# Performance work log

Measured on AMD Instinct MI355X. Metric: run time of the kernel, lower is better.

Reference implementation:

```python
import jax, jax.numpy as jnp
import numpy as np

B, L, D, H, K = 4, 2048, 1024, 16, 3
HEAD_DIM = D // H
LN_EPS = 1e-5


def setup_inputs() -> dict:
    key = jax.random.key(0)
    ks = jax.random.split(key, 12)
    w = lambda k, shp: jax.random.normal(k, shp, jnp.float32) * (shp[-1] ** -0.5)
    return {
        "x": jax.random.normal(ks[0], (B, L, D), jnp.float32),
        "band_importance": jax.random.normal(ks[1], (1, L), jnp.float32) * 0.02,
        "Wq": w(ks[2], (D, D)), "bq": jnp.zeros((D,), jnp.float32),
        "Wk": w(ks[3], (D, D)), "bk": jnp.zeros((D,), jnp.float32),
        "Wv": w(ks[4], (D, D)), "bv": jnp.zeros((D,), jnp.float32),
        "Wo": w(ks[5], (D, D)), "bo": jnp.zeros((D,), jnp.float32),
        "gamma": jnp.ones((D,), jnp.float32),
        "beta": jnp.zeros((D,), jnp.float32),
    }


def reference(x, band_importance, Wq, bq, Wk, bk, Wv, bv, Wo, bo, gamma, beta):
    Bx, Lx, Dx = x.shape
    hd = Dx // H
    # top-k over softmax(band_importance); PyTorch bool attn_mask: True = BLOCKED
    imp = jax.nn.softmax(band_importance, axis=-1)[0]            # (L,)
    _, idx = jax.lax.top_k(imp, K)                               # (K,) int
    col_mask = jnp.zeros((Lx,), bool).at[idx].set(True)          # (L,) True -> masked out
    bias = jnp.where(col_mask, -jnp.inf, 0.0).astype(x.dtype)    # (L,)

    q = (x @ Wq.T + bq).reshape(Bx, Lx, H, hd)
    k_ = (x @ Wk.T + bk).reshape(Bx, Lx, H, hd)
    v = (x @ Wv.T + bv).reshape(Bx, Lx, H, hd)

    scale = 1.0 / np.sqrt(hd)
    scores = jnp.einsum("bqhd,bkhd->bhqk", q, k_) * scale + bias[None, None, None, :]
    attn = jax.nn.softmax(scores, axis=-1)                       # (B,H,L,L)
    ctx = jnp.einsum("bhqk,bkhd->bqhd", attn, v).reshape(Bx, Lx, Dx)
    attn_out = ctx @ Wo.T + bo

    y = x + attn_out                                             # residual
    mu = jnp.mean(y, axis=-1, keepdims=True)
    var = jnp.mean((y - mu) ** 2, axis=-1, keepdims=True)
    return (y - mu) * jax.lax.rsqrt(var + LN_EPS) * gamma + beta
```

## Files before the change

### kernel.cpp

```cpp
#include <hip/hip_runtime.h>

#define GAS __attribute__((address_space(1)))
#define LAS __attribute__((address_space(3)))

typedef __attribute__((ext_vector_type(8))) short short8;
typedef __attribute__((ext_vector_type(4))) float f32x4;
typedef __attribute__((ext_vector_type(16))) float f32x16;
typedef __attribute__((ext_vector_type(4))) unsigned int u32x4;

#define MFMA16(a,b,c) __builtin_amdgcn_mfma_f32_16x16x32_bf16(a,b,c,0,0,0)
#define MFMA32(a,b,c) __builtin_amdgcn_mfma_f32_32x32x16_bf16(a,b,c,0,0,0)

__device__ __forceinline__ unsigned short f2b(float f) {
  unsigned u = __float_as_uint(f);
  u += 0x7fffu + ((u >> 16) & 1u);
  return (unsigned short)(u >> 16);
}
__device__ __forceinline__ float b2f(unsigned short h) {
  return __uint_as_float(((unsigned)h) << 16);
}
__device__ __forceinline__ unsigned cvtpk(float a, float b) {
  unsigned r;
  asm("v_cvt_pk_bf16_f32 %0, %1, %2" : "=v"(r) : "v"(a), "v"(b));
  return r;
}
__device__ __forceinline__ void pl32swap(unsigned &x, unsigned &y) {
  auto r = __builtin_amdgcn_permlane32_swap((int)x, (int)y, false, false);
  x = (unsigned)r[0]; y = (unsigned)r[1];
}
__device__ __forceinline__ float xhalf_sum(float v) {
  auto r = __builtin_amdgcn_permlane32_swap(__float_as_int(v), __float_as_int(v), false, false);
  return __int_as_float(r[0]) + __int_as_float(r[1]);
}
__device__ __forceinline__ float fexp2(float x) {
  float r;
  asm("v_exp_f32 %0, %1" : "=v"(r) : "v"(x));
  return r;
}

union FW { u32x4 u; short8 s; };

__global__ void cvt_all(const float* __restrict__ x,
                        const float* __restrict__ Wq, const float* __restrict__ Wk,
                        const float* __restrict__ Wv, const float* __restrict__ Wo,
                        unsigned short* __restrict__ xb,
                        unsigned short* __restrict__ Wqkvb,
                        unsigned short* __restrict__ Wob) {
  const int bid = blockIdx.x;
  const float* src;
  unsigned short* dst;
  int idx;
  if (bid < 8192) {
    src = x; dst = xb; idx = bid * 256 + threadIdx.x;
  } else {
    int wb = bid - 8192;
    int seg = wb >> 10;
    idx = (wb & 1023) * 256 + threadIdx.x;
    src = (seg == 0) ? Wq : (seg == 1) ? Wk : (seg == 2) ? Wv : Wo;
    dst = (seg == 3) ? Wob : (Wqkvb + (size_t)seg * 1048576);
  }
  float4 v = reinterpret_cast<const float4*>(src)[idx];
  ushort4 o;
  o.x = f2b(v.x); o.y = f2b(v.y); o.z = f2b(v.z); o.w = f2b(v.w);
  reinterpret_cast<ushort4*>(dst)[idx] = o;
}

__global__ void topk_idx(const float* __restrict__ band, int* __restrict__ idxout) {
  __shared__ float svals[256];
  __shared__ int   sidx[256];
  __shared__ int   chosen[3];
  const int t = threadIdx.x;
  for (int pass = 0; pass < 3; ++pass) {
    float best = -INFINITY; int bi = 1 << 30;
    for (int j = t; j < 2048; j += 256) {
      float v = band[j];
      bool skip = false;
      for (int p2 = 0; p2 < pass; ++p2) skip |= (chosen[p2] == j);
      if (!skip && (v > best || (v == best && j < bi))) { best = v; bi = j; }
    }
    svals[t] = best; sidx[t] = bi;
    __syncthreads();
    for (int s = 128; s > 0; s >>= 1) {
      if (t < s) {
        float v2 = svals[t + s]; int i2 = sidx[t + s];
        if (v2 > svals[t] || (v2 == svals[t] && i2 < sidx[t])) { svals[t] = v2; sidx[t] = i2; }
      }
      __syncthreads();
    }
    if (t == 0) chosen[pass] = sidx[0];
    __syncthreads();
  }
  if (t < 3) idxout[t] = chosen[t];
}

__global__ __launch_bounds__(256) void gemm_qkv(
    const unsigned short* __restrict__ A,
    const unsigned short* __restrict__ Wqkv,
    const float* __restrict__ bq, const float* __restrict__ bk,
    const float* __restrict__ bv,
    unsigned short* __restrict__ qout, unsigned short* __restrict__ kout,
    unsigned short* __restrict__ vout, float qscale)
{
  __shared__ short As[128][64];
  __shared__ short Bs[128][64];
  const int tid = threadIdx.x;
  const int w = tid >> 6, lane = tid & 63;
  const int wm = w >> 1, wn = w & 1;
  const int flat = blockIdx.y * 64 + blockIdx.x;
  const int swb = (flat & 7) * 192 + (flat >> 3);
  const int m0 = (swb & 63) * 128, n0 = (swb >> 6) * 128;
  const int rA = lane >> 3, cA = lane & 7;

  const int seg = n0 >> 10;
  const float* biasp = (seg == 0) ? bq : (seg == 1) ? bk : bv;
  unsigned short* outp = (seg == 0) ? qout : (seg == 1) ? kout : vout;
  const float scale = (seg == 0) ? qscale : 1.0f;

  f32x4 acc[4][4];
  #pragma unroll
  for (int mt = 0; mt < 4; ++mt)
    #pragma unroll
    for (int nt = 0; nt < 4; ++nt)
      #pragma unroll
      for (int r = 0; r < 4; ++r) acc[mt][nt][r] = 0.f;

  for (int kt = 0; kt < 16; ++kt) {
    #pragma unroll
    for (int j = 0; j < 4; ++j) {
      int r = w * 32 + j * 8;
      const unsigned short* ga = A + (size_t)(m0 + r + rA) * 1024 + kt * 64 + cA * 8;
      __builtin_amdgcn_global_load_lds((const GAS void*)ga, (LAS void*)&As[r][0], 16, 0, 0);
      const unsigned short* gb = Wqkv + (size_t)(n0 + r + rA) * 1024 + kt * 64 + cA * 8;
      __builtin_amdgcn_global_load_lds((const GAS void*)gb, (LAS void*)&Bs[r][0], 16, 0, 0);
    }
    __syncthreads();
    #pragma unroll
    for (int kc = 0; kc < 2; ++kc) {
      short8 a[4], b[4];
      #pragma unroll
      for (int mt = 0; mt < 4; ++mt)
        a[mt] = *reinterpret_cast<const short8*>(
            &As[wm * 64 + mt * 16 + (lane & 15)][kc * 32 + (lane >> 4) * 8]);
      #pragma unroll
      for (int nt = 0; nt < 4; ++nt)
        b[nt] = *reinterpret_cast<const short8*>(
            &Bs[wn * 64 + nt * 16 + (lane & 15)][kc * 32 + (lane >> 4) * 8]);
      __builtin_amdgcn_s_setprio(1);
      #pragma unroll
      for (int mt = 0; mt < 4; ++mt)
        #pragma unroll
        for (int nt = 0; nt < 4; ++nt)
          acc[mt][nt] = MFMA16(a[mt], b[nt], acc[mt][nt]);
      __builtin_amdgcn_s_setprio(0);
    }
    __syncthreads();
  }
  #pragma unroll
  for (int nt = 0; nt < 4; ++nt) {
    int col = n0 + wn * 64 + nt * 16 + (lane & 15);
    int coll = col & 1023;
    float bval = biasp[coll];
    int h_ = coll >> 6, d_ = coll & 63;
    #pragma unroll
    for (int mt = 0; mt < 4; ++mt) {
      int rbase = m0 + wm * 64 + mt * 16 + ((lane >> 4) << 2);
      #pragma unroll
      for (int r = 0; r < 4; ++r) {
        unsigned short val = f2b((acc[mt][nt][r] + bval) * scale);
        int row = rbase + r;
        int b_ = row >> 11, lt_ = row & 2047;
        outp[(((size_t)(b_ * 16 + h_)) * 2048 + lt_) * 64 + d_] = val;
      }
    }
  }
}

__global__ __launch_bounds__(256) void gemm_wo(
    const unsigned short* __restrict__ A,
    const unsigned short* __restrict__ Bw,
    const float* __restrict__ bias,
    unsigned short* __restrict__ C)
{
  __shared__ short As[128][64];
  __shared__ short Bs[128][64];
  const int tid = threadIdx.x;
  const int w = tid >> 6, lane = tid & 63;
  const int wm = w >> 1, wn = w & 1;
  const int flat = blockIdx.y * 64 + blockIdx.x;
  const int swb = (flat & 7) * 64 + (flat >> 3);
  const int m0 = (swb & 63) * 128, n0 = (swb >> 6) * 128;
  const int rA = lane >> 3, cA = lane & 7;

  f32x4 acc[4][4];
  #pragma unroll
  for (int mt = 0; mt < 4; ++mt)
    #pragma unroll
    for (int nt = 0; nt < 4; ++nt)
      #pragma unroll
      for (int r = 0; r < 4; ++r) acc[mt][nt][r] = 0.f;

  for (int kt = 0; kt < 16; ++kt) {
    #pragma unroll
    for (int j = 0; j < 4; ++j) {
      int r = w * 32 + j * 8;
      const unsigned short* ga = A + (size_t)(m0 + r + rA) * 1024 + kt * 64 + cA * 8;
      __builtin_amdgcn_global_load_lds((const GAS void*)ga, (LAS void*)&As[r][0], 16, 0, 0);
      const unsigned short* gb = Bw + (size_t)(n0 + r + rA) * 1024 + kt * 64 + cA * 8;
      __builtin_amdgcn_global_load_lds((const GAS void*)gb, (LAS void*)&Bs[r][0], 16, 0, 0);
    }
    __syncthreads();
    #pragma unroll
    for (int kc = 0; kc < 2; ++kc) {
      short8 a[4], b[4];
      #pragma unroll
      for (int mt = 0; mt < 4; ++mt)
        a[mt] = *reinterpret_cast<const short8*>(
            &As[wm * 64 + mt * 16 + (lane & 15)][kc * 32 + (lane >> 4) * 8]);
      #pragma unroll
      for (int nt = 0; nt < 4; ++nt)
        b[nt] = *reinterpret_cast<const short8*>(
            &Bs[wn * 64 + nt * 16 + (lane & 15)][kc * 32 + (lane >> 4) * 8]);
      __builtin_amdgcn_s_setprio(1);
      #pragma unroll
      for (int mt = 0; mt < 4; ++mt)
        #pragma unroll
        for (int nt = 0; nt < 4; ++nt)
          acc[mt][nt] = MFMA16(a[mt], b[nt], acc[mt][nt]);
      __builtin_amdgcn_s_setprio(0);
    }
    __syncthreads();
  }
  #pragma unroll
  for (int nt = 0; nt < 4; ++nt) {
    int col = n0 + wn * 64 + nt * 16 + (lane & 15);
    float bval = bias[col];
    #pragma unroll
    for (int mt = 0; mt < 4; ++mt) {
      int rbase = m0 + wm * 64 + mt * 16 + ((lane >> 4) << 2);
      #pragma unroll
      for (int r = 0; r < 4; ++r)
        C[(size_t)(rbase + r) * 1024 + col] = f2b(acc[mt][nt][r] + bval);
    }
  }
}

__global__ __launch_bounds__(256) void transpose_v(
    const unsigned short* __restrict__ vin,
    unsigned short* __restrict__ vout)
{
  __shared__ short T[64 * 64];
  const int lt = blockIdx.x, bh = blockIdx.y;
  const int tid = threadIdx.x;
  #pragma unroll
  for (int p = 0; p < 2; ++p) {
    int id = p * 256 + tid; int l = id >> 3, c = id & 7;
    short8 v = *reinterpret_cast<const short8*>(
        vin + ((size_t)bh * 2048 + lt * 64 + l) * 64 + c * 8);
    *reinterpret_cast<short8*>(&T[l * 64 + ((c ^ (l & 7)) * 8)]) = v;
  }
  __syncthreads();
  #pragma unroll
  for (int p = 0; p < 2; ++p) {
    int id = p * 256 + tid; int d = id >> 3, c2 = id & 7;
    short8 o;
    #pragma unroll
    for (int j = 0; j < 8; ++j) {
      int l = c2 * 8 + j;
      o[j] = T[l * 64 + (((d >> 3) ^ (l & 7)) * 8) + (d & 7)];
    }
    *reinterpret_cast<short8*>(vout + ((size_t)bh * 64 + d) * 2048 + lt * 64 + c2 * 8) = o;
  }
}

#define PACK8(S, j0, OUT) {                                        \
    unsigned A_ = cvtpk(S[(j0)+0], S[(j0)+1]);                     \
    unsigned B_ = cvtpk(S[(j0)+4], S[(j0)+5]);                     \
    unsigned C_ = cvtpk(S[(j0)+2], S[(j0)+3]);                     \
    unsigned D_ = cvtpk(S[(j0)+6], S[(j0)+7]);                     \
    pl32swap(A_, B_); pl32swap(C_, D_);                            \
    FW f_; f_.u[0] = A_; f_.u[1] = C_; f_.u[2] = B_; f_.u[3] = D_; \
    OUT = f_.s; }

__global__ __launch_bounds__(256, 3) void attn4(
    const unsigned short* __restrict__ qg,
    const unsigned short* __restrict__ kg,
    const unsigned short* __restrict__ vtg,
    const int* __restrict__ midx,
    unsigned short* __restrict__ ctx)
{
  __shared__ short Ks[2][64 * 64];
  __shared__ short Vs[2][64 * 64];
  const int tid = threadIdx.x, w = tid >> 6, lane = tid & 63;
  const int flat = blockIdx.y * 16 + blockIdx.x;
  const int swzb = (flat & 7) * 128 + (flat >> 3);
  const int qt = swzb & 15, bh = swzb >> 4;
  const int q0 = qt * 128;
  const int lo5 = lane & 31, hi = lane >> 5;
  const int i0 = midx[0], i1 = midx[1], i2 = midx[2];

  const int qrow = q0 + w * 32 + lo5;
  const unsigned short* qp = qg + ((size_t)bh * 2048 + qrow) * 64 + hi * 8;
  short8 qf[4];
  #pragma unroll
  for (int ds = 0; ds < 4; ++ds) qf[ds] = *reinterpret_cast<const short8*>(qp + ds * 16);

  f32x16 oacc0, oacc1, lacc;
  #pragma unroll
  for (int r = 0; r < 16; ++r) { oacc0[r] = 0.f; oacc1[r] = 0.f; lacc[r] = 0.f; }

  const int swzoff = (((lane & 7) ^ (lane >> 3))) * 8;
  const unsigned short* kp0 =
      kg + ((size_t)bh * 2048 + w * 8 + (lane >> 3)) * 64 + swzoff;
  const unsigned short* kp1 = kp0 + 32 * 64;
  const unsigned short* vp0 =
      vtg + ((size_t)(bh * 64 + w * 8 + (lane >> 3))) * 2048 + swzoff;
  const unsigned short* vp1 = vp0 + 32 * 2048;

#define STAGE_K(bufi, tt) do {                                                 \
    __builtin_amdgcn_global_load_lds((const GAS void*)(kp0 + (tt) * 4096),     \
        (LAS void*)&Ks[bufi][(w * 8) * 64], 16, 0, 0);                         \
    __builtin_amdgcn_global_load_lds((const GAS void*)(kp1 + (tt) * 4096),     \
        (LAS void*)&Ks[bufi][(32 + w * 8) * 64], 16, 0, 0);                    \
  } while (0)
#define STAGE_V(bufi, tt) do {                                                 \
    __builtin_amdgcn_global_load_lds((const GAS void*)(vp0 + (tt) * 64),       \
        (LAS void*)&Vs[bufi][(w * 8) * 64], 16, 0, 0);                         \
    __builtin_amdgcn_global_load_lds((const GAS void*)(vp1 + (tt) * 64),       \
        (LAS void*)&Vs[bufi][(32 + w * 8) * 64], 16, 0, 0);                    \
  } while (0)

  STAGE_K(0, 0); STAGE_V(0, 0);
  STAGE_K(1, 1); STAGE_V(1, 1);

  for (int t = 0; t < 32; ++t) {
    const int buf = t & 1;
    if (t < 31) { asm volatile("s_waitcnt vmcnt(4)" ::: "memory"); }
    else        { asm volatile("s_waitcnt vmcnt(0)" ::: "memory"); }
    __builtin_amdgcn_sched_barrier(0);
    __builtin_amdgcn_s_barrier();
    __builtin_amdgcn_sched_barrier(0);

    short8 kf[8];
    #pragma unroll
    for (int ds = 0; ds < 4; ++ds) {
      int cw = ds * 2 + hi;
      kf[2 * ds] = *reinterpret_cast<const short8*>(
          &Ks[buf][lo5 * 64 + ((cw ^ (lo5 & 7)) * 8)]);
      kf[2 * ds + 1] = *reinterpret_cast<const short8*>(
          &Ks[buf][(32 + lo5) * 64 + ((cw ^ (lo5 & 7)) * 8)]);
    }
    asm volatile("s_waitcnt lgkmcnt(0)" ::: "memory");
    __builtin_amdgcn_sched_barrier(0);
    __builtin_amdgcn_s_barrier();
    __builtin_amdgcn_sched_barrier(0);
    if (t < 30) STAGE_K(buf, t + 2);

    f32x16 s0, s1;
    #pragma unroll
    for (int r = 0; r < 16; ++r) { s0[r] = 0.f; s1[r] = 0.f; }
    __builtin_amdgcn_s_setprio(1);
    #pragma unroll
    for (int ds = 0; ds < 4; ++ds) {
      s0 = MFMA32(kf[2 * ds], qf[ds], s0);
      s1 = MFMA32(kf[2 * ds + 1], qf[ds], s1);
    }
    __builtin_amdgcn_s_setprio(0);

    #pragma unroll
    for (int r = 0; r < 16; ++r) s0[r] = fexp2(s0[r]);
    #pragma unroll
    for (int r = 0; r < 16; ++r) s1[r] = fexp2(s1[r]);

    int t64 = t * 64;
    bool tm = ((unsigned)(i0 - t64) < 64u) | ((unsigned)(i1 - t64) < 64u) |
              ((unsigned)(i2 - t64) < 64u);
    if (tm) {
      #pragma unroll
      for (int r = 0; r < 16; ++r) {
        int kg0 = t64 + (r & 3) + 8 * (r >> 2) + 4 * hi;
        int kg1 = kg0 + 32;
        if (kg0 == i0 || kg0 == i1 || kg0 == i2) s0[r] = 0.f;
        if (kg1 == i0 || kg1 == i1 || kg1 == i2) s1[r] = 0.f;
      }
    }

    #pragma unroll
    for (int r = 0; r < 16; ++r) lacc[r] += s0[r] + s1[r];

    short8 pa[4];
    PACK8(s0, 0, pa[0]); PACK8(s0, 8, pa[1]);
    PACK8(s1, 0, pa[2]); PACK8(s1, 8, pa[3]);

    short8 vf[8];
    #pragma unroll
    for (int ks = 0; ks < 4; ++ks) {
      int cw = ks * 2 + hi;
      vf[2 * ks] = *reinterpret_cast<const short8*>(
          &Vs[buf][lo5 * 64 + ((cw ^ (lo5 & 7)) * 8)]);
      vf[2 * ks + 1] = *reinterpret_cast<const short8*>(
          &Vs[buf][(32 + lo5) * 64 + ((cw ^ (lo5 & 7)) * 8)]);
    }
    asm volatile("s_waitcnt lgkmcnt(0)" ::: "memory");
    __builtin_amdgcn_sched_barrier(0);
    __builtin_amdgcn_s_barrier();
    __builtin_amdgcn_sched_barrier(0);
    if (t < 30) STAGE_V(buf, t + 2);

    __builtin_amdgcn_s_setprio(1);
    #pragma unroll
    for (int ks = 0; ks < 4; ++ks) {
      oacc0 = MFMA32(pa[ks], vf[2 * ks], oacc0);
      oacc1 = MFMA32(pa[ks], vf[2 * ks + 1], oacc1);
    }
    __builtin_amdgcn_s_setprio(0);
  }

  float lsum = 0.f;
  #pragma unroll
  for (int r = 0; r < 16; ++r) lsum += lacc[r];
  lsum = xhalf_sum(lsum);
  const int bb = bh >> 4, hh = bh & 15;
  float rinv = 1.0f / lsum;
  #pragma unroll
  for (int r = 0; r < 16; ++r) {
    int row = (r & 3) + 8 * (r >> 2) + 4 * hi;
    float rv = __int_as_float(__builtin_amdgcn_ds_bpermute(
        (row + (lane & 32)) * 4, __float_as_int(rinv)));
    int qr = q0 + w * 32 + row;
    size_t base = (((size_t)(bb * 2048 + qr)) * 16 + hh) * 64;
    ctx[base + lo5]      = f2b(oacc0[r] * rv);
    ctx[base + 32 + lo5] = f2b(oacc1[r] * rv);
  }
}

__global__ __launch_bounds__(256) void resid_ln(
    const float* __restrict__ x, const unsigned short* __restrict__ ao,
    const float* __restrict__ gamma, const float* __restrict__ beta,
    float* __restrict__ out)
{
  const int row = blockIdx.x, t = threadIdx.x;
  const size_t base = (size_t)row * 1024;
  float4 xv = reinterpret_cast<const float4*>(x + base)[t];
  ushort4 av = reinterpret_cast<const ushort4*>(ao + base)[t];
  float y[4] = {xv.x + b2f(av.x), xv.y + b2f(av.y), xv.z + b2f(av.z), xv.w + b2f(av.w)};
  float sum = y[0] + y[1] + y[2] + y[3];
  float sq = y[0] * y[0] + y[1] * y[1] + y[2] * y[2] + y[3] * y[3];
  #pragma unroll
  for (int off = 1; off < 64; off <<= 1) {
    sum += __shfl_xor(sum, off);
    sq += __shfl_xor(sq, off);
  }
  __shared__ float s1[4], s2[4];
  int w = t >> 6, lane = t & 63;
  if (lane == 0) { s1[w] = sum; s2[w] = sq; }
  __syncthreads();
  sum = s1[0] + s1[1] + s1[2] + s1[3];
  sq = s2[0] + s2[1] + s2[2] + s2[3];
  float mu = sum * (1.f / 1024.f);
  float var = sq * (1.f / 1024.f) - mu * mu;
  float inv = rsqrtf(var + 1e-5f);
  float4 gv = reinterpret_cast<const float4*>(gamma)[t];
  float4 bv = reinterpret_cast<const float4*>(beta)[t];
  float4 o;
  o.x = (y[0] - mu) * inv * gv.x + bv.x;
  o.y = (y[1] - mu) * inv * gv.y + bv.y;
  o.z = (y[2] - mu) * inv * gv.z + bv.z;
  o.w = (y[3] - mu) * inv * gv.w + bv.w;
  reinterpret_cast<float4*>(out + base)[t] = o;
}

extern "C" void kernel_launch(void* const* d_in, const int* in_sizes, int n_in,
                              void* d_out, int out_size, void* d_ws, size_t ws_size,
                              hipStream_t stream)
{
  const float* x     = (const float*)d_in[0];
  const float* band  = (const float*)d_in[1];
  const float* Wq    = (const float*)d_in[2];
  const float* bq    = (const float*)d_in[3];
  const float* Wk    = (const float*)d_in[4];
  const float* bk    = (const float*)d_in[5];
  const float* Wv    = (const float*)d_in[6];
  const float* bv    = (const float*)d_in[7];
  const float* Wo    = (const float*)d_in[8];
  const float* bo    = (const float*)d_in[9];
  const float* gamma = (const float*)d_in[10];
  const float* beta  = (const float*)d_in[11];
  float* out = (float*)d_out;

  char* ws = (char*)d_ws;
  int*            idxw  = (int*)(ws);
  unsigned short* xb    = (unsigned short*)(ws + 4096);
  unsigned short* Wqkvb = (unsigned short*)(ws + 16781312);
  unsigned short* Wob   = (unsigned short*)(ws + 23072768);
  unsigned short* qb    = (unsigned short*)(ws + 25169920);
  unsigned short* kb    = (unsigned short*)(ws + 41947136);
  unsigned short* vhb   = (unsigned short*)(ws + 58724352);
  unsigned short* vtb   = (unsigned short*)(ws + 75501568);
  unsigned short* ctxb  = vhb;
  unsigned short* aob   = qb;

  const float QSCALE = 0.125f * 1.44269504f;

  cvt_all<<<12288, 256, 0, stream>>>(x, Wq, Wk, Wv, Wo, xb, Wqkvb, Wob);
  topk_idx<<<1, 256, 0, stream>>>(band, idxw);

  gemm_qkv<<<dim3(64, 24), 256, 0, stream>>>(xb, Wqkvb, bq, bk, bv,
                                             qb, kb, vhb, QSCALE);

  transpose_v<<<dim3(32, 64), 256, 0, stream>>>(vhb, vtb);

  attn4<<<dim3(16, 64), 256, 0, stream>>>(qb, kb, vtb, idxw, ctxb);

  gemm_wo<<<dim3(64, 8), 256, 0, stream>>>(ctxb, Wob, bo, aob);

  resid_ln<<<8192, 256, 0, stream>>>(x, aob, gamma, beta, out);
}
```

Baseline: 232.4 us.

## Double query rows per attention wave, fuse V transpose and topk launches

Each attention wave now handles 64 query rows as two 32-row sets against every staged K/V tile, doubling reuse of the K and V fragments loaded from LDS. The grid is halved and the occupancy hint drops from 3 to 2 because of the larger register footprint. The QKV GEMM epilogue writes V straight into the transposed layout, which removes the separate transpose kernel and its round trip through memory. The top-k selection is merged into the conversion kernel as one extra block, saving a launch.

```diff
diff --git a/kernel.cpp b/kernel.cpp
--- a/kernel.cpp
+++ b/kernel.cpp
@@ -37,35 +37,40 @@
   asm("v_exp_f32 %0, %1" : "=v"(r) : "v"(x));
   return r;
 }
+__device__ __forceinline__ short8 ld8(const unsigned short* p) {
+  return *reinterpret_cast<const short8*>(p);
+}
 
 union FW { u32x4 u; short8 s; };
 
-__global__ void cvt_all(const float* __restrict__ x,
-                        const float* __restrict__ Wq, const float* __restrict__ Wk,
-                        const float* __restrict__ Wv, const float* __restrict__ Wo,
-                        unsigned short* __restrict__ xb,
-                        unsigned short* __restrict__ Wqkvb,
-                        unsigned short* __restrict__ Wob) {
+__global__ void cvt_topk(const float* __restrict__ x,
+                         const float* __restrict__ Wq, const float* __restrict__ Wk,
+                         const float* __restrict__ Wv, const float* __restrict__ Wo,
+                         const float* __restrict__ band,
+                         unsigned short* __restrict__ xb,
+                         unsigned short* __restrict__ Wqkvb,
+                         unsigned short* __restrict__ Wob,
+                         int* __restrict__ idxout) {
   const int bid = blockIdx.x;
-  const float* src;
-  unsigned short* dst;
-  int idx;
-  if (bid < 8192) {
-    src = x; dst = xb; idx = bid * 256 + threadIdx.x;
-  } else {
-    int wb = bid - 8192;
-    int seg = wb >> 10;
-    idx = (wb & 1023) * 256 + threadIdx.x;
-    src = (seg == 0) ? Wq : (seg == 1) ? Wk : (seg == 2) ? Wv : Wo;
-    dst = (seg == 3) ? Wob : (Wqkvb + (size_t)seg * 1048576);
-  }
-  float4 v = reinterpret_cast<const float4*>(src)[idx];
-  ushort4 o;
-  o.x = f2b(v.x); o.y = f2b(v.y); o.z = f2b(v.z); o.w = f2b(v.w);
-  reinterpret_cast<ushort4*>(dst)[idx] = o;
-}
-
-__global__ void topk_idx(const float* __restrict__ band, int* __restrict__ idxout) {
+  if (bid < 12288) {
+    const float* src;
+    unsigned short* dst;
+    int idx;
+    if (bid < 8192) {
+      src = x; dst = xb; idx = bid * 256 + threadIdx.x;
+    } else {
+      int wb = bid - 8192;
+      int seg = wb >> 10;
+      idx = (wb & 1023) * 256 + threadIdx.x;
+      src = (seg == 0) ? Wq : (seg == 1) ? Wk : (seg == 2) ? Wv : Wo;
+      dst = (seg == 3) ? Wob : (Wqkvb + (size_t)seg * 1048576);
+    }
+    float4 v = reinterpret_cast<const float4*>(src)[idx];
+    ushort4 o;
+    o.x = f2b(v.x); o.y = f2b(v.y); o.z = f2b(v.z); o.w = f2b(v.w);
+    reinterpret_cast<ushort4*>(dst)[idx] = o;
+    return;
+  }
   __shared__ float svals[256];
   __shared__ int   sidx[256];
   __shared__ int   chosen[3];
@@ -99,7 +104,7 @@
     const float* __restrict__ bq, const float* __restrict__ bk,
     const float* __restrict__ bv,
     unsigned short* __restrict__ qout, unsigned short* __restrict__ kout,
-    unsigned short* __restrict__ vout, float qscale)
+    unsigned short* __restrict__ vtout, float qscale)
 {
   __shared__ short As[128][64];
   __shared__ short Bs[128][64];
@@ -113,7 +118,6 @@
 
   const int seg = n0 >> 10;
   const float* biasp = (seg == 0) ? bq : (seg == 1) ? bk : bv;
-  unsigned short* outp = (seg == 0) ? qout : (seg == 1) ? kout : vout;
   const float scale = (seg == 0) ? qscale : 1.0f;
 
   f32x4 acc[4][4];
@@ -155,21 +159,43 @@
     }
     __syncthreads();
   }
-  #pragma unroll
-  for (int nt = 0; nt < 4; ++nt) {
-    int col = n0 + wn * 64 + nt * 16 + (lane & 15);
-    int coll = col & 1023;
-    float bval = biasp[coll];
-    int h_ = coll >> 6, d_ = coll & 63;
-    #pragma unroll
-    for (int mt = 0; mt < 4; ++mt) {
-      int rbase = m0 + wm * 64 + mt * 16 + ((lane >> 4) << 2);
-      #pragma unroll
-      for (int r = 0; r < 4; ++r) {
-        unsigned short val = f2b((acc[mt][nt][r] + bval) * scale);
-        int row = rbase + r;
-        int b_ = row >> 11, lt_ = row & 2047;
-        outp[(((size_t)(b_ * 16 + h_)) * 2048 + lt_) * 64 + d_] = val;
+
+  if (seg == 2) {
+    #pragma unroll
+    for (int nt = 0; nt < 4; ++nt) {
+      int coll = (n0 + wn * 64 + nt * 16 + (lane & 15)) & 1023;
+      float bval = biasp[coll];
+      int h_ = coll >> 6, d_ = coll & 63;
+      #pragma unroll
+      for (int mt = 0; mt < 4; ++mt) {
+        int rbase = m0 + wm * 64 + mt * 16 + ((lane >> 4) << 2);
+        int b_ = rbase >> 11, lt_ = rbase & 2047;
+        ushort4 pk;
+        pk.x = f2b(acc[mt][nt][0] + bval);
+        pk.y = f2b(acc[mt][nt][1] + bval);
+        pk.z = f2b(acc[mt][nt][2] + bval);
+        pk.w = f2b(acc[mt][nt][3] + bval);
+        *reinterpret_cast<ushort4*>(
+            &vtout[(((size_t)(b_ * 16 + h_)) * 64 + d_) * 2048 + lt_]) = pk;
+      }
+    }
+  } else {
+    unsigned short* outp = (seg == 0) ? qout : kout;
+    #pragma unroll
+    for (int nt = 0; nt < 4; ++nt) {
+      int coll = (n0 + wn * 64 + nt * 16 + (lane & 15)) & 1023;
+      float bval = biasp[coll];
+      int h_ = coll >> 6, d_ = coll & 63;
+      #pragma unroll
+      for (int mt = 0; mt < 4; ++mt) {
+        int rbase = m0 + wm * 64 + mt * 16 + ((lane >> 4) << 2);
+        #pragma unroll
+        for (int r = 0; r < 4; ++r) {
+          unsigned short val = f2b((acc[mt][nt][r] + bval) * scale);
+          int row = rbase + r;
+          int b_ = row >> 11, lt_ = row & 2047;
+          outp[(((size_t)(b_ * 16 + h_)) * 2048 + lt_) * 64 + d_] = val;
+        }
       }
     }
   }
@@ -244,34 +270,6 @@
   }
 }
 
-__global__ __launch_bounds__(256) void transpose_v(
-    const unsigned short* __restrict__ vin,
-    unsigned short* __restrict__ vout)
-{
-  __shared__ short T[64 * 64];
-  const int lt = blockIdx.x, bh = blockIdx.y;
-  const int tid = threadIdx.x;
-  #pragma unroll
-  for (int p = 0; p < 2; ++p) {
-    int id = p * 256 + tid; int l = id >> 3, c = id & 7;
-    short8 v = *reinterpret_cast<const short8*>(
-        vin + ((size_t)bh * 2048 + lt * 64 + l) * 64 + c * 8);
-    *reinterpret_cast<short8*>(&T[l * 64 + ((c ^ (l & 7)) * 8)]) = v;
-  }
-  __syncthreads();
-  #pragma unroll
-  for (int p = 0; p < 2; ++p) {
-    int id = p * 256 + tid; int d = id >> 3, c2 = id & 7;
-    short8 o;
-    #pragma unroll
-    for (int j = 0; j < 8; ++j) {
-      int l = c2 * 8 + j;
-      o[j] = T[l * 64 + (((d >> 3) ^ (l & 7)) * 8) + (d & 7)];
-    }
-    *reinterpret_cast<short8*>(vout + ((size_t)bh * 64 + d) * 2048 + lt * 64 + c2 * 8) = o;
-  }
-}
-
 #define PACK8(S, j0, OUT) {                                        \
     unsigned A_ = cvtpk(S[(j0)+0], S[(j0)+1]);                     \
     unsigned B_ = cvtpk(S[(j0)+4], S[(j0)+5]);                     \
@@ -281,7 +279,7 @@
     FW f_; f_.u[0] = A_; f_.u[1] = C_; f_.u[2] = B_; f_.u[3] = D_; \
     OUT = f_.s; }
 
-__global__ __launch_bounds__(256, 3) void attn4(
+__global__ __launch_bounds__(256, 2) void attn6(
     const unsigned short* __restrict__ qg,
     const unsigned short* __restrict__ kg,
     const unsigned short* __restrict__ vtg,
@@ -291,22 +289,31 @@
   __shared__ short Ks[2][64 * 64];
   __shared__ short Vs[2][64 * 64];
   const int tid = threadIdx.x, w = tid >> 6, lane = tid & 63;
-  const int flat = blockIdx.y * 16 + blockIdx.x;
-  const int swzb = (flat & 7) * 128 + (flat >> 3);
-  const int qt = swzb & 15, bh = swzb >> 4;
-  const int q0 = qt * 128;
+  const int flat = blockIdx.y * 8 + blockIdx.x;
+  const int swzb = (flat & 7) * 64 + (flat >> 3);
+  const int qt = swzb & 7, bh = swzb >> 3;
+  const int q0 = qt * 256;
   const int lo5 = lane & 31, hi = lane >> 5;
   const int i0 = midx[0], i1 = midx[1], i2 = midx[2];
 
-  const int qrow = q0 + w * 32 + lo5;
-  const unsigned short* qp = qg + ((size_t)bh * 2048 + qrow) * 64 + hi * 8;
-  short8 qf[4];
-  #pragma unroll
-  for (int ds = 0; ds < 4; ++ds) qf[ds] = *reinterpret_cast<const short8*>(qp + ds * 16);
-
-  f32x16 oacc0, oacc1, lacc;
-  #pragma unroll
-  for (int r = 0; r < 16; ++r) { oacc0[r] = 0.f; oacc1[r] = 0.f; lacc[r] = 0.f; }
+  const int qra = q0 + w * 64 + lo5;
+  const unsigned short* qpa = qg + ((size_t)bh * 2048 + qra) * 64 + hi * 8;
+  const unsigned short* qpb = qpa + (size_t)32 * 64;
+  short8 qfa[4], qfb[4];
+  #pragma unroll
+  for (int ds = 0; ds < 4; ++ds) {
+    qfa[ds] = ld8(qpa + ds * 16);
+    qfb[ds] = ld8(qpb + ds * 16);
+  }
+
+  f32x16 oacc0a, oacc1a, oacc0b, oacc1b;
+  f32x4 lacca, laccb;
+  #pragma unroll
+  for (int r = 0; r < 16; ++r) {
+    oacc0a[r] = 0.f; oacc1a[r] = 0.f; oacc0b[r] = 0.f; oacc1b[r] = 0.f;
+  }
+  #pragma unroll
+  for (int r = 0; r < 4; ++r) { lacca[r] = 0.f; laccb[r] = 0.f; }
 
   const int swzoff = (((lane & 7) ^ (lane >> 3))) * 8;
   const unsigned short* kp0 =
@@ -361,8 +368,8 @@
     __builtin_amdgcn_s_setprio(1);
     #pragma unroll
     for (int ds = 0; ds < 4; ++ds) {
-      s0 = MFMA32(kf[2 * ds], qf[ds], s0);
-      s1 = MFMA32(kf[2 * ds + 1], qf[ds], s1);
+      s0 = MFMA32(kf[2 * ds], qfa[ds], s0);
+      s1 = MFMA32(kf[2 * ds + 1], qfa[ds], s1);
     }
     __builtin_amdgcn_s_setprio(0);
 
@@ -371,9 +378,9 @@
     #pragma unroll
     for (int r = 0; r < 16; ++r) s1[r] = fexp2(s1[r]);
 
-    int t64 = t * 64;
-    bool tm = ((unsigned)(i0 - t64) < 64u) | ((unsigned)(i1 - t64) < 64u) |
-              ((unsigned)(i2 - t64) < 64u);
+    const int t64 = t * 64;
+    const bool tm = ((unsigned)(i0 - t64) < 64u) | ((unsigned)(i1 - t64) < 64u) |
+                    ((unsigned)(i2 - t64) < 64u);
     if (tm) {
       #pragma unroll
       for (int r = 0; r < 16; ++r) {
@@ -383,13 +390,22 @@
         if (kg1 == i0 || kg1 == i1 || kg1 == i2) s1[r] = 0.f;
       }
     }
-
-    #pragma unroll
-    for (int r = 0; r < 16; ++r) lacc[r] += s0[r] + s1[r];
-
-    short8 pa[4];
-    PACK8(s0, 0, pa[0]); PACK8(s0, 8, pa[1]);
-    PACK8(s1, 0, pa[2]); PACK8(s1, 8, pa[3]);
+    #pragma unroll
+    for (int r = 0; r < 16; ++r) lacca[r & 3] += s0[r] + s1[r];
+
+    short8 paa0, paa1, paa2, paa3;
+    PACK8(s0, 0, paa0); PACK8(s0, 8, paa1);
+    PACK8(s1, 0, paa2); PACK8(s1, 8, paa3);
+
+    #pragma unroll
+    for (int r = 0; r < 16; ++r) { s0[r] = 0.f; s1[r] = 0.f; }
+    __builtin_amdgcn_s_setprio(1);
+    #pragma unroll
+    for (int ds = 0; ds < 4; ++ds) {
+      s0 = MFMA32(kf[2 * ds], qfb[ds], s0);
+      s1 = MFMA32(kf[2 * ds + 1], qfb[ds], s1);
+    }
+    __builtin_amdgcn_s_setprio(0);
 
     short8 vf[8];
     #pragma unroll
@@ -400,6 +416,27 @@
       vf[2 * ks + 1] = *reinterpret_cast<const short8*>(
           &Vs[buf][(32 + lo5) * 64 + ((cw ^ (lo5 & 7)) * 8)]);
     }
+
+    #pragma unroll
+    for (int r = 0; r < 16; ++r) s0[r] = fexp2(s0[r]);
+    #pragma unroll
+    for (int r = 0; r < 16; ++r) s1[r] = fexp2(s1[r]);
+    if (tm) {
+      #pragma unroll
+      for (int r = 0; r < 16; ++r) {
+        int kg0 = t64 + (r & 3) + 8 * (r >> 2) + 4 * hi;
+        int kg1 = kg0 + 32;
+        if (kg0 == i0 || kg0 == i1 || kg0 == i2) s0[r] = 0.f;
+        if (kg1 == i0 || kg1 == i1 || kg1 == i2) s1[r] = 0.f;
+      }
+    }
+    #pragma unroll
+    for (int r = 0; r < 16; ++r) laccb[r & 3] += s0[r] + s1[r];
+
+    short8 pab0, pab1, pab2, pab3;
+    PACK8(s0, 0, pab0); PACK8(s0, 8, pab1);
+    PACK8(s1, 0, pab2); PACK8(s1, 8, pab3);
+
     asm volatile("s_waitcnt lgkmcnt(0)" ::: "memory");
     __builtin_amdgcn_sched_barrier(0);
     __builtin_amdgcn_s_barrier();
@@ -407,29 +444,36 @@
     if (t < 30) STAGE_V(buf, t + 2);
 
     __builtin_amdgcn_s_setprio(1);
-    #pragma unroll
-    for (int ks = 0; ks < 4; ++ks) {
-      oacc0 = MFMA32(pa[ks], vf[2 * ks], oacc0);
-      oacc1 = MFMA32(pa[ks], vf[2 * ks + 1], oacc1);
-    }
+    oacc0a = MFMA32(paa0, vf[0], oacc0a); oacc1a = MFMA32(paa0, vf[1], oacc1a);
+    oacc0b = MFMA32(pab0, vf[0], oacc0b); oacc1b = MFMA32(pab0, vf[1], oacc1b);
+    oacc0a = MFMA32(paa1, vf[2], oacc0a); oacc1a = MFMA32(paa1, vf[3], oacc1a);
+    oacc0b = MFMA32(pab1, vf[2], oacc0b); oacc1b = MFMA32(pab1, vf[3], oacc1b);
+    oacc0a = MFMA32(paa2, vf[4], oacc0a); oacc1a = MFMA32(paa2, vf[5], oacc1a);
+    oacc0b = MFMA32(pab2, vf[4], oacc0b); oacc1b = MFMA32(pab2, vf[5], oacc1b);
+    oacc0a = MFMA32(paa3, vf[6], oacc0a); oacc1a = MFMA32(paa3, vf[7], oacc1a);
+    oacc0b = MFMA32(pab3, vf[6], oacc0b); oacc1b = MFMA32(pab3, vf[7], oacc1b);
     __builtin_amdgcn_s_setprio(0);
   }
 
-  float lsum = 0.f;
-  #pragma unroll
-  for (int r = 0; r < 16; ++r) lsum += lacc[r];
-  lsum = xhalf_sum(lsum);
+  float lsa = lacca[0] + lacca[1] + lacca[2] + lacca[3];
+  float lsb = laccb[0] + laccb[1] + laccb[2] + laccb[3];
+  lsa = xhalf_sum(lsa);
+  lsb = xhalf_sum(lsb);
   const int bb = bh >> 4, hh = bh & 15;
-  float rinv = 1.0f / lsum;
+  float rinva = 1.0f / lsa, rinvb = 1.0f / lsb;
   #pragma unroll
   for (int r = 0; r < 16; ++r) {
     int row = (r & 3) + 8 * (r >> 2) + 4 * hi;
-    float rv = __int_as_float(__builtin_amdgcn_ds_bpermute(
-        (row + (lane & 32)) * 4, __float_as_int(rinv)));
-    int qr = q0 + w * 32 + row;
-    size_t base = (((size_t)(bb * 2048 + qr)) * 16 + hh) * 64;
-    ctx[base + lo5]      = f2b(oacc0[r] * rv);
-    ctx[base + 32 + lo5] = f2b(oacc1[r] * rv);
+    int addr = (row + (lane & 32)) * 4;
+    float rva = __int_as_float(__builtin_amdgcn_ds_bpermute(addr, __float_as_int(rinva)));
+    float rvb = __int_as_float(__builtin_amdgcn_ds_bpermute(addr, __float_as_int(rinvb)));
+    int qr = q0 + w * 64 + row;
+    size_t basea = (((size_t)(bb * 2048 + qr)) * 16 + hh) * 64;
+    size_t baseb = (((size_t)(bb * 2048 + qr + 32)) * 16 + hh) * 64;
+    ctx[basea + lo5]      = f2b(oacc0a[r] * rva);
+    ctx[basea + 32 + lo5] = f2b(oacc1a[r] * rva);
+    ctx[baseb + lo5]      = f2b(oacc0b[r] * rvb);
+    ctx[baseb + 32 + lo5] = f2b(oacc1b[r] * rvb);
   }
 }
 
@@ -494,22 +538,18 @@
   unsigned short* Wob   = (unsigned short*)(ws + 23072768);
   unsigned short* qb    = (unsigned short*)(ws + 25169920);
   unsigned short* kb    = (unsigned short*)(ws + 41947136);
-  unsigned short* vhb   = (unsigned short*)(ws + 58724352);
+  unsigned short* ctxb  = (unsigned short*)(ws + 58724352);
   unsigned short* vtb   = (unsigned short*)(ws + 75501568);
-  unsigned short* ctxb  = vhb;
   unsigned short* aob   = qb;
 
   const float QSCALE = 0.125f * 1.44269504f;
 
-  cvt_all<<<12288, 256, 0, stream>>>(x, Wq, Wk, Wv, Wo, xb, Wqkvb, Wob);
-  topk_idx<<<1, 256, 0, stream>>>(band, idxw);
+  cvt_topk<<<12289, 256, 0, stream>>>(x, Wq, Wk, Wv, Wo, band, xb, Wqkvb, Wob, idxw);
 
   gemm_qkv<<<dim3(64, 24), 256, 0, stream>>>(xb, Wqkvb, bq, bk, bv,
-                                             qb, kb, vhb, QSCALE);
-
-  transpose_v<<<dim3(32, 64), 256, 0, stream>>>(vhb, vtb);
-
-  attn4<<<dim3(16, 64), 256, 0, stream>>>(qb, kb, vtb, idxw, ctxb);
+                                             qb, kb, vtb, QSCALE);
+
+  attn6<<<dim3(8, 64), 256, 0, stream>>>(qb, kb, vtb, idxw, ctxb);
 
   gemm_wo<<<dim3(64, 8), 256, 0, stream>>>(ctxb, Wob, bo, aob);
 
```

After: 281.2 us. +21.0%, slower.
